# Kernel optimization log

Measured on AMD Instinct MI355X. Metric: run time of the kernel, lower is better.

The kernel has to match this reference:

```python
import jax, jax.numpy as jnp
import numpy as np

B, SEQ, ENC = 128, 1024, 64
D, SEG = 512, 64
SNX = SEQ // SEG   # 16 encoder segments
PRED = 512
SNY = PRED // SEG  # 8 decoder segments


def setup_inputs() -> dict:
    key = jax.random.key(0)
    ks = jax.random.split(key, 18)
    s = 0.05
    r = lambda k, shape: jax.random.normal(k, shape, jnp.float32) * s
    return {
        "x": jax.random.normal(ks[0], (B, SEQ, ENC), jnp.float32),
        # valueEmbedding: Linear(seg_len -> d_model) + SiLU
        "W_emb": r(ks[1], (D, SEG)), "b_emb": r(ks[2], (D,)),
        # GRUCell (encoder residual path)
        "cell_Wih": r(ks[3], (3 * D, D)), "cell_Whh": r(ks[4], (3 * D, D)),
        "cell_bih": r(ks[5], (3 * D,)), "cell_bhh": r(ks[6], (3 * D,)),
        # nn.GRU (decoder, single layer, single step)
        "gru_Wih": r(ks[7], (3 * D, D)), "gru_Whh": r(ks[8], (3 * D, D)),
        "gru_bih": r(ks[9], (3 * D,)), "gru_bhh": r(ks[10], (3 * D,)),
        # residual_projection: Linear(d_model -> d_model)
        "res_W": r(ks[11], (D, D)), "res_b": r(ks[12], (D,)),
        # positional / channel embeddings (each hidden//2)
        "pos_emb": jax.random.normal(ks[13], (SNY, D // 2), jnp.float32),
        "channel_emb": jax.random.normal(ks[14], (ENC, D // 2), jnp.float32),
        # predict: Linear(d_model -> seg_len)
        "pred_W": r(ks[15], (SEG, D)), "pred_b": r(ks[16], (SEG,)),
    }


def gru_step(x_t, h, Wih, Whh, bih, bhh):
    """Single torch-convention GRU step. x_t,h: (N,D)."""
    gx = x_t @ Wih.T + bih          # (N, 3D)
    gh = h @ Whh.T + bhh            # (N, 3D)
    xr, xz, xn = jnp.split(gx, 3, axis=-1)
    hr, hz, hn = jnp.split(gh, 3, axis=-1)
    rg = jax.nn.sigmoid(xr + hr)
    zg = jax.nn.sigmoid(xz + hz)
    ng = jnp.tanh(xn + rg * hn)
    return (1.0 - zg) * ng + zg * h


def reference(x, W_emb, b_emb, cell_Wih, cell_Whh, cell_bih, cell_bhh,
              gru_Wih, gru_Whh, gru_bih, gru_bhh, res_W, res_b,
              pos_emb, channel_emb, pred_W, pred_b):
    seq_last = jax.lax.stop_gradient(x[:, -1:, :])          # (B,1,ENC)
    xs = (x - seq_last).transpose(0, 2, 1).reshape(-1, SNX, SEG)  # (B*ENC, SNX, SEG)
    emb = jax.nn.silu(xs @ W_emb.T + b_emb)                 # (N, SNX, D)
    N = emb.shape[0]

    def step(h, x_t):
        h_cell = gru_step(x_t, h, cell_Wih, cell_Whh, cell_bih, cell_bhh)
        h_new = x_t + (h_cell @ res_W.T + res_b)            # residual projection
        return h_new, None

    h0 = jnp.zeros((N, D), emb.dtype)
    hn, _ = jax.lax.scan(step, h0, jnp.swapaxes(emb, 0, 1))  # hn: (N, D)

    # decoder inputs: [pos_emb | channel_emb] laid out (ENC, SNY, D), tiled over batch
    half = D // 2
    pe = jnp.concatenate([
        jnp.broadcast_to(pos_emb[None, :, :], (ENC, SNY, half)),
        jnp.broadcast_to(channel_emb[:, None, :], (ENC, SNY, half)),
    ], axis=-1).reshape(-1, D)                               # (ENC*SNY, D)
    pe = jnp.tile(pe, (B, 1))                                # (B*ENC*SNY, D)
    h0d = jnp.repeat(hn, SNY, axis=0)                        # (B*ENC*SNY, D)

    hy = gru_step(pe, h0d, gru_Wih, gru_Whh, gru_bih, gru_bhh)  # 1-step GRU decode
    y = hy @ pred_W.T + pred_b                               # (B*ENC*SNY, SEG)
    y = y.reshape(B, ENC, PRED).transpose(0, 2, 1)           # (B, PRED, ENC)
    return y + seq_last
```

## Files before the change

kernel.cpp:

```cpp
#include <hip/hip_runtime.h>
#include <stdint.h>

#define DEV __device__ __forceinline__

typedef __bf16 bf16x8 __attribute__((ext_vector_type(8)));
typedef float  f32x4  __attribute__((ext_vector_type(4)));


DEV unsigned short f2bf(float f){
  union { float f; uint32_t u; } v; v.f = f;
  uint32_t r = (v.u + 0x7FFFu + ((v.u >> 16) & 1u)) >> 16;
  return (unsigned short)r;
}
DEV float bf2f(unsigned short s){
  union { uint32_t u; float f; } v; v.u = ((uint32_t)s) << 16; return v.f;
}
DEV float sigm(float x){
  return __builtin_amdgcn_rcpf(1.0f + __builtin_amdgcn_exp2f(-1.442695041f*x));
}
DEV float tanhe(float x){
  return 1.0f - 2.0f*__builtin_amdgcn_rcpf(__builtin_amdgcn_exp2f(2.885390082f*x) + 1.0f);
}

#define AS1(p) ((const __attribute__((address_space(1))) uint32_t*)(p))
#define AS3(p) ((__attribute__((address_space(3))) uint32_t*)(p))

template<int NROWS, int NW>
DEV void gstage(const unsigned short* src, int ld, unsigned short* lds, int tid){
  constexpr int CH = NROWS/8;
  constexpr int PW = CH/NW;
  int wid = tid >> 6, lane = tid & 63;
  int rsub = lane >> 3;
  int slot = (lane & 7) ^ rsub;
  #pragma unroll
  for (int r = 0; r < PW; r++){
    int chunk = wid*PW + r;
    int row = chunk*8 + rsub;
    __builtin_amdgcn_global_load_lds(AS1(src + (size_t)row*ld + slot*8),
                                     AS3(lds + chunk*512), 16, 0, 0);
  }
}

DEV void zero24(f32x4 (&a)[2][4]){
  f32x4 z = {0.f,0.f,0.f,0.f};
  #pragma unroll
  for (int m = 0; m < 2; m++)
    #pragma unroll
    for (int n = 0; n < 4; n++) a[m][n] = z;
}
DEV void zero22(f32x4 (&a)[2][2]){
  f32x4 z = {0.f,0.f,0.f,0.f};
  #pragma unroll
  for (int m = 0; m < 2; m++)
    #pragma unroll
    for (int n = 0; n < 2; n++) a[m][n] = z;
}

DEV void mmaW(const unsigned short* As, const unsigned short* Bs, int wm0,
              int lane, f32x4 (&acc)[2][4]){
  int lr = lane & 15, lk = (lane >> 4)*8, sw = (lane & 7) << 3;
  #pragma unroll
  for (int ks = 0; ks < 2; ks++){
    int ko = (ks*32 + lk) ^ sw;
    bf16x8 a[2], b[4];
    #pragma unroll
    for (int m = 0; m < 2; m++)
      a[m] = *reinterpret_cast<const bf16x8*>(&As[(wm0 + m*16 + lr)*64 + ko]);
    #pragma unroll
    for (int n = 0; n < 4; n++)
      b[n] = *reinterpret_cast<const bf16x8*>(&Bs[(n*16 + lr)*64 + ko]);
    #pragma unroll
    for (int m = 0; m < 2; m++)
      #pragma unroll
      for (int n = 0; n < 4; n++)
        acc[m][n] = __builtin_amdgcn_mfma_f32_16x16x32_bf16(a[m], b[n], acc[m][n], 0, 0, 0);
  }
}

DEV void mmaWc(const unsigned short* As, const unsigned short* Bs, int wm0,
               int lane, f32x4 (&acc)[2][2]){
  int lr = lane & 15, lk = (lane >> 4)*8, sw = (lane & 7) << 3;
  #pragma unroll
  for (int ks = 0; ks < 2; ks++){
    int ko = (ks*32 + lk) ^ sw;
    bf16x8 a[2], b[2];
    #pragma unroll
    for (int m = 0; m < 2; m++)
      a[m] = *reinterpret_cast<const bf16x8*>(&As[(wm0 + m*16 + lr)*64 + ko]);
    #pragma unroll
    for (int n = 0; n < 2; n++)
      b[n] = *reinterpret_cast<const bf16x8*>(&Bs[(n*16 + lr)*64 + ko]);
    #pragma unroll
    for (int m = 0; m < 2; m++)
      #pragma unroll
      for (int n = 0; n < 2; n++)
        acc[m][n] = __builtin_amdgcn_mfma_f32_16x16x32_bf16(a[m], b[n], acc[m][n], 0, 0, 0);
  }
}

DEV void mmaW3c(const unsigned short* As, const unsigned short* Bs, int wm0,
                int lane, f32x4 (&a1)[2][2], f32x4 (&a2)[2][2], f32x4 (&a3)[2][2]){
  int lr = lane & 15, lk = (lane >> 4)*8, sw = (lane & 7) << 3;
  #pragma unroll
  for (int ks = 0; ks < 2; ks++){
    int ko = (ks*32 + lk) ^ sw;
    bf16x8 a[2], b[2];
    #pragma unroll
    for (int m = 0; m < 2; m++)
      a[m] = *reinterpret_cast<const bf16x8*>(&As[(wm0 + m*16 + lr)*64 + ko]);
    #pragma unroll
    for (int n = 0; n < 2; n++)
      b[n] = *reinterpret_cast<const bf16x8*>(&Bs[(n*16 + lr)*64 + ko]);
    #pragma unroll
    for (int m = 0; m < 2; m++)
      #pragma unroll
      for (int n = 0; n < 2; n++)
        a1[m][n] = __builtin_amdgcn_mfma_f32_16x16x32_bf16(a[m], b[n], a1[m][n], 0, 0, 0);
    #pragma unroll
    for (int n = 0; n < 2; n++)
      b[n] = *reinterpret_cast<const bf16x8*>(&Bs[2048 + (n*16 + lr)*64 + ko]);
    #pragma unroll
    for (int m = 0; m < 2; m++)
      #pragma unroll
      for (int n = 0; n < 2; n++)
        a2[m][n] = __builtin_amdgcn_mfma_f32_16x16x32_bf16(a[m], b[n], a2[m][n], 0, 0, 0);
    #pragma unroll
    for (int n = 0; n < 2; n++)
      b[n] = *reinterpret_cast<const bf16x8*>(&Bs[4096 + (n*16 + lr)*64 + ko]);
    #pragma unroll
    for (int m = 0; m < 2; m++)
      #pragma unroll
      for (int n = 0; n < 2; n++)
        a3[m][n] = __builtin_amdgcn_mfma_f32_16x16x32_bf16(a[m], b[n], a3[m][n], 0, 0, 0);
  }
}

DEV void kloopS(const unsigned short* A0, const unsigned short* B0,
                unsigned short* As, unsigned short* Bs,
                int tid, int wm0, int lane, f32x4 (&acc)[2][4]){
  for (int kt = 0; kt < 8; kt++){
    gstage<128,4>(A0 + kt*64, 512, As, tid);
    gstage<64,4>(B0 + kt*64, 512, Bs, tid);
    __syncthreads();
    mmaW(As, Bs, wm0, lane, acc);
    __syncthreads();
  }
}

__global__ __launch_bounds__(256) void cvt_all_kernel(
    const float* cWih, const float* cWhh, const float* gWih, const float* gWhh,
    const float* resW, const float* predW, const float* Wemb,
    unsigned short* o0, unsigned short* o1, unsigned short* o2, unsigned short* o3,
    unsigned short* o4, unsigned short* o5, unsigned short* o6){
  int g = blockIdx.x*256 + threadIdx.x;
  const float* s; unsigned short* d; int idx;
  if      (g < 196608){ s=cWih;  d=o0; idx=g; }
  else if (g < 393216){ s=cWhh;  d=o1; idx=g-196608; }
  else if (g < 589824){ s=gWih;  d=o2; idx=g-393216; }
  else if (g < 786432){ s=gWhh;  d=o3; idx=g-589824; }
  else if (g < 851968){ s=resW;  d=o4; idx=g-786432; }
  else if (g < 860160){ s=predW; d=o5; idx=g-851968; }
  else if (g < 868352){ s=Wemb;  d=o6; idx=g-860160; }
  else return;
  float4 v = reinterpret_cast<const float4*>(s)[idx];
  ushort4 r; r.x=f2bf(v.x); r.y=f2bf(v.y); r.z=f2bf(v.z); r.w=f2bf(v.w);
  reinterpret_cast<ushort4*>(d)[idx] = r;
}

__global__ __launch_bounds__(256) void build_pe_kernel(const float* pos, const float* chan, unsigned short* pe){
  int i = blockIdx.x*256 + threadIdx.x;
  if (i >= 512*512) return;
  int m = i >> 9, d = i & 511;
  int c = m >> 3, sy = m & 7;
  float v = (d < 256) ? pos[sy*256 + d] : chan[c*256 + (d-256)];
  pe[i] = f2bf(v);
}

__global__ __launch_bounds__(256) void xs_kernel(const float* __restrict__ x,
                                                 unsigned short* __restrict__ xs){
  __shared__ float tile[64][65];
  __shared__ float lastv[64];
  int b = blockIdx.y, tk0 = blockIdx.x*64, tid = threadIdx.x;
  if (tid < 64) lastv[tid] = x[(size_t)b*65536 + 65472 + tid];
  #pragma unroll
  for (int k = 0; k < 16; k++){
    int id = tid + k*256;
    int i = id >> 6, c = id & 63;
    tile[i][c] = x[(size_t)b*65536 + (size_t)(tk0+i)*64 + c];
  }
  __syncthreads();
  #pragma unroll
  for (int k = 0; k < 16; k++){
    int id = tid + k*256;
    int c = id >> 6, i = id & 63;
    xs[(size_t)(b*64 + c)*1024 + tk0 + i] = f2bf(tile[i][c] - lastv[c]);
  }
}

__global__ __launch_bounds__(256) void embed_kernel(const unsigned short* __restrict__ xs,
    const unsigned short* __restrict__ wemb, const float* __restrict__ bemb,
    unsigned short* __restrict__ embout, int t0, size_t zs){
  __shared__ unsigned short As[8192];
  __shared__ unsigned short Bs[4096];
  int tid = threadIdx.x, lane = tid & 63, wid = tid >> 6, wm0 = wid*32;
  int rA0 = blockIdx.x*128, d0 = blockIdx.y*64;
  int t = t0 + blockIdx.z;
  unsigned short* out = embout + (size_t)blockIdx.z * zs;

  gstage<128,4>(xs + (size_t)rA0*1024 + t*64, 1024, As, tid);
  gstage<64,4>(wemb + (size_t)d0*64, 64, Bs, tid);
  __syncthreads();
  f32x4 acc[2][4]; zero24(acc);
  mmaW(As, Bs, wm0, lane, acc);

  int lr = lane & 15, lj = (lane >> 4)*4;
  #pragma unroll
  for (int m = 0; m < 2; m++)
    #pragma unroll
    for (int n = 0; n < 4; n++){
      int col = d0 + n*16 + lr;
      float bb = bemb[col];
      #pragma unroll
      for (int j = 0; j < 4; j++){
        int row = rA0 + wm0 + m*16 + lj + j;
        float v = acc[m][n][j] + bb;
        v = v * sigm(v);
        out[(size_t)row*512 + col] = f2bf(v);
      }
    }
}

__global__ __launch_bounds__(256,4) void gates_kernel(
    const unsigned short* __restrict__ emb, const unsigned short* __restrict__ hbf,
    const unsigned short* __restrict__ Wih, const unsigned short* __restrict__ Whh,
    const float* __restrict__ bih, const float* __restrict__ bhh,
    unsigned short* __restrict__ hcell){
  __shared__ unsigned short As[8192];
  __shared__ unsigned short Bs[3*2048];
  int tid = threadIdx.x, lane = tid & 63, wid = tid >> 6, wm0 = wid*32;
  int id = blockIdx.x;
  int g = (id & 7) + ((id >> 7) << 3);
  int c = (id >> 3) & 15;
  int rA0 = g*128, d0 = c*32;

  f32x4 aR[2][2], aZ[2][2], aNx[2][2], aNh[2][2];
  zero22(aR); zero22(aZ); zero22(aNx); zero22(aNh);

  {
    const unsigned short* A = emb + (size_t)rA0*512;
    const unsigned short* BR = Wih + (size_t)d0*512;
    const unsigned short* BZ = Wih + (size_t)(512 + d0)*512;
    const unsigned short* BN = Wih + (size_t)(1024 + d0)*512;
    for (int kt = 0; kt < 8; kt++){
      gstage<128,4>(A + kt*64, 512, As, tid);
      gstage<32,4>(BR + kt*64, 512, Bs, tid);
      gstage<32,4>(BZ + kt*64, 512, Bs + 2048, tid);
      gstage<32,4>(BN + kt*64, 512, Bs + 4096, tid);
      __syncthreads();
      mmaW3c(As, Bs, wm0, lane, aR, aZ, aNx);
      __syncthreads();
    }
  }
  {
    const unsigned short* A = hbf + (size_t)rA0*512;
    const unsigned short* BR = Whh + (size_t)d0*512;
    const unsigned short* BZ = Whh + (size_t)(512 + d0)*512;
    const unsigned short* BN = Whh + (size_t)(1024 + d0)*512;
    for (int kt = 0; kt < 8; kt++){
      gstage<128,4>(A + kt*64, 512, As, tid);
      gstage<32,4>(BR + kt*64, 512, Bs, tid);
      gstage<32,4>(BZ + kt*64, 512, Bs + 2048, tid);
      gstage<32,4>(BN + kt*64, 512, Bs + 4096, tid);
      __syncthreads();
      mmaW3c(As, Bs, wm0, lane, aR, aZ, aNh);
      __syncthreads();
    }
  }

  int lr = lane & 15, lj = (lane >> 4)*4;
  #pragma unroll
  for (int n = 0; n < 2; n++){
    int col = d0 + n*16 + lr;
    float brr = bih[col] + bhh[col];
    float bzz = bih[512 + col] + bhh[512 + col];
    float bni = bih[1024 + col], bnh = bhh[1024 + col];
    #pragma unroll
    for (int m = 0; m < 2; m++)
      #pragma unroll
      for (int j = 0; j < 4; j++){
        int row = rA0 + wm0 + m*16 + lj + j;
        float rg = sigm(aR[m][n][j] + brr);
        float zg = sigm(aZ[m][n][j] + bzz);
        float ng = tanhe(aNx[m][n][j] + bni + rg*(aNh[m][n][j] + bnh));
        float h  = bf2f(hbf[(size_t)row*512 + col]);
        hcell[(size_t)row*512 + col] = f2bf((1.0f - zg)*ng + zg*h);
      }
  }
}

__global__ __launch_bounds__(256,4) void res_kernel(
    const unsigned short* __restrict__ hcell, const unsigned short* __restrict__ Wres,
    const float* __restrict__ res_b, const unsigned short* __restrict__ emb,
    unsigned short* __restrict__ hbf){
  __shared__ unsigned short As[8192];
  __shared__ unsigned short Bs[2048];
  int tid = threadIdx.x, lane = tid & 63, wid = tid >> 6, wm0 = wid*32;
  int id = blockIdx.x;
  int g = (id & 7) + ((id >> 7) << 3);
  int c = (id >> 3) & 15;
  int rA0 = g*128, d0 = c*32;

  f32x4 acc[2][2]; zero22(acc);
  const unsigned short* A = hcell + (size_t)rA0*512;
  const unsigned short* Bw = Wres + (size_t)d0*512;
  for (int kt = 0; kt < 8; kt++){
    gstage<128,4>(A + kt*64, 512, As, tid);
    gstage<32,4>(Bw + kt*64, 512, Bs, tid);
    __syncthreads();
    mmaWc(As, Bs, wm0, lane, acc);
    __syncthreads();
  }

  int lr = lane & 15, lj = (lane >> 4)*4;
  #pragma unroll
  for (int n = 0; n < 2; n++){
    int col = d0 + n*16 + lr;
    float bb = res_b[col];
    #pragma unroll
    for (int m = 0; m < 2; m++)
      #pragma unroll
      for (int j = 0; j < 4; j++){
        int row = rA0 + wm0 + m*16 + lj + j;
        float v = acc[m][n][j] + bb + bf2f(emb[(size_t)row*512 + col]);
        hbf[(size_t)row*512 + col] = f2bf(v);
      }
  }
}

template<bool BF16OUT>
__global__ __launch_bounds__(256) void gemm_bias_kernel(
    const unsigned short* __restrict__ A, const unsigned short* __restrict__ B,
    const float* __restrict__ bias, float* __restrict__ Cf,
    unsigned short* __restrict__ Cb, int Nld){
  __shared__ unsigned short As[8192];
  __shared__ unsigned short Bs[4096];
  int tid = threadIdx.x, lane = tid & 63, wid = tid >> 6, wm0 = wid*32;
  int rA0 = blockIdx.x*128, rB0 = blockIdx.y*64;

  f32x4 acc[2][4]; zero24(acc);
  kloopS(A + (size_t)rA0*512, B + (size_t)rB0*512, As, Bs, tid, wm0, lane, acc);

  int lr = lane & 15, lj = (lane >> 4)*4;
  #pragma unroll
  for (int m = 0; m < 2; m++)
    #pragma unroll
    for (int n = 0; n < 4; n++){
      int col = rB0 + n*16 + lr;
      float bb = bias[col];
      #pragma unroll
      for (int j = 0; j < 4; j++){
        int row = rA0 + wm0 + m*16 + lj + j;
        float v = acc[m][n][j] + bb;
        if (BF16OUT) Cb[(size_t)row*Nld + col] = f2bf(v);
        else         Cf[(size_t)row*Nld + col] = v;
      }
    }
}

DEV void bf8ld(const unsigned short* p, float* o){
  uint4 u = *reinterpret_cast<const uint4*>(p);
  union { uint32_t w; float f; } v;
  v.w = u.x << 16;          o[0] = v.f;
  v.w = u.x & 0xffff0000u;  o[1] = v.f;
  v.w = u.y << 16;          o[2] = v.f;
  v.w = u.y & 0xffff0000u;  o[3] = v.f;
  v.w = u.z << 16;          o[4] = v.f;
  v.w = u.z & 0xffff0000u;  o[5] = v.f;
  v.w = u.w << 16;          o[6] = v.f;
  v.w = u.w & 0xffff0000u;  o[7] = v.f;
}

__global__ __launch_bounds__(256) void hy_kernel(const float* __restrict__ gxd,
    const unsigned short* __restrict__ ghd, const unsigned short* __restrict__ hb,
    unsigned short* __restrict__ hy){
  int gid = blockIdx.x*256 + threadIdx.x;
  #pragma unroll 1
  for (int it = 0; it < 8; it++, gid += 2048*256){
    int r = gid >> 6, dg = gid & 63;
    int n = r >> 3, sy = r & 7, c = n & 63, mpe = c*8 + sy;
    int d = dg*8;
    const float* gx = gxd + (size_t)mpe*1536 + d;
    const unsigned short* gh = ghd + (size_t)n*1536 + d;
    const unsigned short* hh = hb + (size_t)n*512 + d;
    float4 xr0 = *reinterpret_cast<const float4*>(gx);
    float4 xr1 = *reinterpret_cast<const float4*>(gx + 4);
    float4 xz0 = *reinterpret_cast<const float4*>(gx + 512);
    float4 xz1 = *reinterpret_cast<const float4*>(gx + 516);
    float4 xn0 = *reinterpret_cast<const float4*>(gx + 1024);
    float4 xn1 = *reinterpret_cast<const float4*>(gx + 1028);
    float xr[8] = {xr0.x,xr0.y,xr0.z,xr0.w,xr1.x,xr1.y,xr1.z,xr1.w};
    float xz[8] = {xz0.x,xz0.y,xz0.z,xz0.w,xz1.x,xz1.y,xz1.z,xz1.w};
    float xn[8] = {xn0.x,xn0.y,xn0.z,xn0.w,xn1.x,xn1.y,xn1.z,xn1.w};
    float hr[8], hz[8], hn[8], h[8];
    bf8ld(gh, hr); bf8ld(gh + 512, hz); bf8ld(gh + 1024, hn); bf8ld(hh, h);
    unsigned short w[8];
    #pragma unroll
    for (int j = 0; j < 8; j++){
      float rg = sigm(xr[j] + hr[j]);
      float zg = sigm(xz[j] + hz[j]);
      float ng = tanhe(xn[j] + rg*hn[j]);
      w[j] = f2bf((1.0f - zg)*ng + zg*h[j]);
    }
    *reinterpret_cast<uint4*>(hy + (size_t)r*512 + d) =
        *reinterpret_cast<const uint4*>(w);
  }
}

__global__ __launch_bounds__(256) void pred_kernel(
    const unsigned short* __restrict__ hy, const unsigned short* __restrict__ predW,
    const float* __restrict__ predb, const float* __restrict__ x,
    float* __restrict__ out){
  __shared__ unsigned short As[8192];
  __shared__ unsigned short Bs[4096];
  int tid = threadIdx.x, lane = tid & 63, wid = tid >> 6, wm0 = wid*32;
  int rA0 = blockIdx.x*128;

  f32x4 acc[2][4]; zero24(acc);
  kloopS(hy + (size_t)rA0*512, predW, As, Bs, tid, wm0, lane, acc);

  int lr = lane & 15, lj = (lane >> 4)*4;
  #pragma unroll
  for (int n = 0; n < 4; n++){
    int s = n*16 + lr;
    float bb = predb[s];
    #pragma unroll
    for (int m = 0; m < 2; m++)
      #pragma unroll
      for (int j = 0; j < 4; j++){
        int r = rA0 + wm0 + m*16 + lj + j;
        int nn = r >> 3, sy = r & 7, b = nn >> 6, c = nn & 63;
        out[(size_t)b*32768 + (size_t)(sy*64 + s)*64 + c] =
            acc[m][n][j] + bb + x[(size_t)b*65536 + 65472 + c];
      }
  }
}

extern "C" void kernel_launch(void* const* d_in, const int* in_sizes, int n_in,
                              void* d_out, int out_size, void* d_ws, size_t ws_size,
                              hipStream_t stream){
  (void)in_sizes; (void)n_in; (void)out_size;
  const float* x     = (const float*)d_in[0];
  const float* Wemb  = (const float*)d_in[1];
  const float* bemb  = (const float*)d_in[2];
  const float* cWih  = (const float*)d_in[3];
  const float* cWhh  = (const float*)d_in[4];
  const float* cbih  = (const float*)d_in[5];
  const float* cbhh  = (const float*)d_in[6];
  const float* gWih  = (const float*)d_in[7];
  const float* gWhh  = (const float*)d_in[8];
  const float* gbih  = (const float*)d_in[9];
  const float* gbhh  = (const float*)d_in[10];
  const float* resW  = (const float*)d_in[11];
  const float* resb  = (const float*)d_in[12];
  const float* pos   = (const float*)d_in[13];
  const float* chan  = (const float*)d_in[14];
  const float* predW = (const float*)d_in[15];
  const float* predb = (const float*)d_in[16];
  float* out = (float*)d_out;

  uint8_t* ws = (uint8_t*)d_ws;
  size_t o = 0;
  auto take = [&](size_t bytes){ uint8_t* p = ws + o; o += (bytes + 255) & ~(size_t)255; return p; };
  unsigned short* wb_cWih  = (unsigned short*)take(786432*2);
  unsigned short* wb_cWhh  = (unsigned short*)take(786432*2);
  unsigned short* wb_gWih  = (unsigned short*)take(786432*2);
  unsigned short* wb_gWhh  = (unsigned short*)take(786432*2);
  unsigned short* wb_resW  = (unsigned short*)take(262144*2);
  unsigned short* wb_predW = (unsigned short*)take(32768*2);
  unsigned short* wb_Wemb  = (unsigned short*)take(32768*2);
  unsigned short* pe_bf    = (unsigned short*)take(262144*2);
  unsigned short* h_bf     = (unsigned short*)take(4194304*2);

  uint8_t* U = ws + o;
  unsigned short* xs_all = (unsigned short*)(U);
  unsigned short* hcell  = (unsigned short*)(U + 16777216);
  unsigned short* emb    = (unsigned short*)(U + 25165824);
  unsigned short* ghd    = (unsigned short*)(U);
  float*          gxd    = (float*)(U + 25165824);
  unsigned short* hy     = (unsigned short*)(U + 28311552);

  bool big = ws_size >= o + (size_t)25165824 + (size_t)16*8388608;
  size_t zs = big ? 4194304 : 0;

  cvt_all_kernel<<<3392, 256, 0, stream>>>(cWih, cWhh, gWih, gWhh, resW, predW, Wemb,
      wb_cWih, wb_cWhh, wb_gWih, wb_gWhh, wb_resW, wb_predW, wb_Wemb);
  build_pe_kernel<<<1024, 256, 0, stream>>>(pos, chan, pe_bf);
  xs_kernel<<<dim3(16, 128), 256, 0, stream>>>(x, xs_all);
  hipMemsetAsync(h_bf, 0, (size_t)4194304*2, stream);

  if (big)
    embed_kernel<<<dim3(64, 8, 16), 256, 0, stream>>>(xs_all, wb_Wemb, bemb, emb, 0, zs);

  for (int t = 0; t < 16; t++){
    const unsigned short* emb_t = emb + (big ? (size_t)t*4194304 : 0);
    if (!big)
      embed_kernel<<<dim3(64, 8, 1), 256, 0, stream>>>(xs_all, wb_Wemb, bemb,
                                                       (unsigned short*)emb_t, t, 0);
    gates_kernel<<<1024, 256, 0, stream>>>(emb_t, h_bf, wb_cWih, wb_cWhh,
                                           cbih, cbhh, hcell);
    res_kernel<<<1024, 256, 0, stream>>>(hcell, wb_resW, resb, emb_t, h_bf);
  }

  gemm_bias_kernel<true><<<dim3(64, 24), 256, 0, stream>>>(h_bf, wb_gWhh, gbhh,
                                                           nullptr, ghd, 1536);
  gemm_bias_kernel<false><<<dim3(4, 24), 256, 0, stream>>>(pe_bf, wb_gWih, gbih,
                                                           gxd, nullptr, 1536);
  hy_kernel<<<2048, 256, 0, stream>>>(gxd, ghd, h_bf, hy);
  pred_kernel<<<512, 256, 0, stream>>>(hy, wb_predW, predb, x, out);
}
```

Before: 761.7 us.

## Fuse decoder GRU gate math into prediction GEMM and raise occupancy bounds

Removes the separate hy_kernel and computes the decoder GRU output inside the prediction GEMM. Each block writes its bf16 hy tile straight into swizzled shared memory before the MFMA step, so the 64K×512 bf16 hy buffer is never written to or read back from global memory. The launch_bounds minimum-blocks hint also rises for gates_kernel (4 to 5) and res_kernel (4 to 7), which may limit registers and cause spills. The fused kernel has only 512 blocks doing the elementwise work, so that work is less parallel than in the old 2048-block kernel.

```diff
diff --git a/kernel.cpp b/kernel.cpp
--- a/kernel.cpp
+++ b/kernel.cpp
@@ -230,7 +230,7 @@
     }
 }
 
-__global__ __launch_bounds__(256,4) void gates_kernel(
+__global__ __launch_bounds__(256,5) void gates_kernel(
     const unsigned short* __restrict__ emb, const unsigned short* __restrict__ hbf,
     const unsigned short* __restrict__ Wih, const unsigned short* __restrict__ Whh,
     const float* __restrict__ bih, const float* __restrict__ bhh,
@@ -298,7 +298,7 @@
   }
 }
 
-__global__ __launch_bounds__(256,4) void res_kernel(
+__global__ __launch_bounds__(256,7) void res_kernel(
     const unsigned short* __restrict__ hcell, const unsigned short* __restrict__ Wres,
     const float* __restrict__ res_b, const unsigned short* __restrict__ emb,
     unsigned short* __restrict__ hbf){
@@ -380,44 +380,9 @@
   v.w = u.w & 0xffff0000u;  o[7] = v.f;
 }
 
-__global__ __launch_bounds__(256) void hy_kernel(const float* __restrict__ gxd,
-    const unsigned short* __restrict__ ghd, const unsigned short* __restrict__ hb,
-    unsigned short* __restrict__ hy){
-  int gid = blockIdx.x*256 + threadIdx.x;
-  #pragma unroll 1
-  for (int it = 0; it < 8; it++, gid += 2048*256){
-    int r = gid >> 6, dg = gid & 63;
-    int n = r >> 3, sy = r & 7, c = n & 63, mpe = c*8 + sy;
-    int d = dg*8;
-    const float* gx = gxd + (size_t)mpe*1536 + d;
-    const unsigned short* gh = ghd + (size_t)n*1536 + d;
-    const unsigned short* hh = hb + (size_t)n*512 + d;
-    float4 xr0 = *reinterpret_cast<const float4*>(gx);
-    float4 xr1 = *reinterpret_cast<const float4*>(gx + 4);
-    float4 xz0 = *reinterpret_cast<const float4*>(gx + 512);
-    float4 xz1 = *reinterpret_cast<const float4*>(gx + 516);
-    float4 xn0 = *reinterpret_cast<const float4*>(gx + 1024);
-    float4 xn1 = *reinterpret_cast<const float4*>(gx + 1028);
-    float xr[8] = {xr0.x,xr0.y,xr0.z,xr0.w,xr1.x,xr1.y,xr1.z,xr1.w};
-    float xz[8] = {xz0.x,xz0.y,xz0.z,xz0.w,xz1.x,xz1.y,xz1.z,xz1.w};
-    float xn[8] = {xn0.x,xn0.y,xn0.z,xn0.w,xn1.x,xn1.y,xn1.z,xn1.w};
-    float hr[8], hz[8], hn[8], h[8];
-    bf8ld(gh, hr); bf8ld(gh + 512, hz); bf8ld(gh + 1024, hn); bf8ld(hh, h);
-    unsigned short w[8];
-    #pragma unroll
-    for (int j = 0; j < 8; j++){
-      float rg = sigm(xr[j] + hr[j]);
-      float zg = sigm(xz[j] + hz[j]);
-      float ng = tanhe(xn[j] + rg*hn[j]);
-      w[j] = f2bf((1.0f - zg)*ng + zg*h[j]);
-    }
-    *reinterpret_cast<uint4*>(hy + (size_t)r*512 + d) =
-        *reinterpret_cast<const uint4*>(w);
-  }
-}
-
-__global__ __launch_bounds__(256) void pred_kernel(
-    const unsigned short* __restrict__ hy, const unsigned short* __restrict__ predW,
+__global__ __launch_bounds__(256) void pred_fused_kernel(
+    const float* __restrict__ gxd, const unsigned short* __restrict__ ghd,
+    const unsigned short* __restrict__ hb, const unsigned short* __restrict__ predW,
     const float* __restrict__ predb, const float* __restrict__ x,
     float* __restrict__ out){
   __shared__ unsigned short As[8192];
@@ -425,8 +390,49 @@
   int tid = threadIdx.x, lane = tid & 63, wid = tid >> 6, wm0 = wid*32;
   int rA0 = blockIdx.x*128;
 
+  int rl = tid >> 1, q = tid & 1;
+  int r = rA0 + rl;
+  int nn = r >> 3, sy = r & 7, cc = nn & 63, mpe = cc*8 + sy;
+  (void)sy;
+  const float* gx = gxd + (size_t)mpe*1536;
+  const unsigned short* gh = ghd + (size_t)nn*1536;
+  const unsigned short* hh = hb + (size_t)nn*512;
+
   f32x4 acc[2][4]; zero24(acc);
-  kloopS(hy + (size_t)rA0*512, predW, As, Bs, tid, wm0, lane, acc);
+
+  for (int kt = 0; kt < 8; kt++){
+    #pragma unroll
+    for (int s = 0; s < 4; s++){
+      int dq = kt*64 + q*32 + s*8;
+      float4 xa = *reinterpret_cast<const float4*>(gx + dq);
+      float4 xb = *reinterpret_cast<const float4*>(gx + dq + 4);
+      float4 za = *reinterpret_cast<const float4*>(gx + 512 + dq);
+      float4 zb = *reinterpret_cast<const float4*>(gx + 516 + dq);
+      float4 na = *reinterpret_cast<const float4*>(gx + 1024 + dq);
+      float4 nb = *reinterpret_cast<const float4*>(gx + 1028 + dq);
+      float xr[8] = {xa.x,xa.y,xa.z,xa.w,xb.x,xb.y,xb.z,xb.w};
+      float xz[8] = {za.x,za.y,za.z,za.w,zb.x,zb.y,zb.z,zb.w};
+      float xn[8] = {na.x,na.y,na.z,na.w,nb.x,nb.y,nb.z,nb.w};
+      float hr[8], hz[8], hn[8], h[8];
+      bf8ld(gh + dq, hr); bf8ld(gh + 512 + dq, hz);
+      bf8ld(gh + 1024 + dq, hn); bf8ld(hh + dq, h);
+      unsigned short w[8];
+      #pragma unroll
+      for (int j = 0; j < 8; j++){
+        float rg = sigm(xr[j] + hr[j]);
+        float zg = sigm(xz[j] + hz[j]);
+        float ng = tanhe(xn[j] + rg*hn[j]);
+        w[j] = f2bf((1.0f - zg)*ng + zg*h[j]);
+      }
+      int slot = (q*4 + s) ^ (rl & 7);
+      *reinterpret_cast<uint4*>(&As[rl*64 + slot*8]) =
+          *reinterpret_cast<const uint4*>(w);
+    }
+    gstage<64,4>(predW + kt*64, 512, Bs, tid);
+    __syncthreads();
+    mmaW(As, Bs, wm0, lane, acc);
+    __syncthreads();
+  }
 
   int lr = lane & 15, lj = (lane >> 4)*4;
   #pragma unroll
@@ -437,10 +443,10 @@
     for (int m = 0; m < 2; m++)
       #pragma unroll
       for (int j = 0; j < 4; j++){
-        int r = rA0 + wm0 + m*16 + lj + j;
-        int nn = r >> 3, sy = r & 7, b = nn >> 6, c = nn & 63;
-        out[(size_t)b*32768 + (size_t)(sy*64 + s)*64 + c] =
-            acc[m][n][j] + bb + x[(size_t)b*65536 + 65472 + c];
+        int rr = rA0 + wm0 + m*16 + lj + j;
+        int n2 = rr >> 3, sy2 = rr & 7, b = n2 >> 6, c2 = n2 & 63;
+        out[(size_t)b*32768 + (size_t)(sy2*64 + s)*64 + c2] =
+            acc[m][n][j] + bb + x[(size_t)b*65536 + 65472 + c2];
       }
   }
 }
@@ -487,7 +493,6 @@
   unsigned short* emb    = (unsigned short*)(U + 25165824);
   unsigned short* ghd    = (unsigned short*)(U);
   float*          gxd    = (float*)(U + 25165824);
-  unsigned short* hy     = (unsigned short*)(U + 28311552);
 
   bool big = ws_size >= o + (size_t)25165824 + (size_t)16*8388608;
   size_t zs = big ? 4194304 : 0;
@@ -515,6 +520,5 @@
                                                            nullptr, ghd, 1536);
   gemm_bias_kernel<false><<<dim3(4, 24), 256, 0, stream>>>(pe_bf, wb_gWih, gbih,
                                                            gxd, nullptr, 1536);
-  hy_kernel<<<2048, 256, 0, stream>>>(gxd, ghd, h_bf, hy);
-  pred_kernel<<<512, 256, 0, stream>>>(hy, wb_predW, predb, x, out);
-}
+  pred_fused_kernel<<<512, 256, 0, stream>>>(gxd, ghd, h_bf, wb_predW, predb, x, out);
+}
```

After: 1.060 ms. 39.2% more time.
